# Kernel tuning notes

Hardware: AMD Instinct MI355X
Metric: run time of the kernel (lower is better)

## Reference

```python
import jax, jax.numpy as jnp
import numpy as np

FORGET_BIAS = 1.0  # tf LSTMCell default

def _lstm_step(c, h, xt, W, b):
    # tf LSTMCell: gates = [x, h] @ W + b, split order (i, j, f, o)
    gates = jnp.concatenate([xt, h], axis=-1) @ W + b
    i, j, f, o = jnp.split(gates, 4, axis=-1)
    c_new = c * jax.nn.sigmoid(f + FORGET_BIAS) + jax.nn.sigmoid(i) * jnp.tanh(j)
    h_new = jnp.tanh(c_new) * jax.nn.sigmoid(o)
    return c_new, h_new

def setup_inputs() -> dict:
    key = jax.random.key(0)
    k1, k2, k3 = jax.random.split(key, 3)
    B, T, H = 512, 1024, 64
    x = jax.random.normal(k1, (B, T, 1), dtype=jnp.float32)
    W1 = jax.random.normal(k2, (1 + H, 4 * H), dtype=jnp.float32) * 0.1
    b1 = jnp.zeros((4 * H,), dtype=jnp.float32)
    W2 = jax.random.normal(k3, (H + 1, 4 * 1), dtype=jnp.float32) * 0.1
    b2 = jnp.zeros((4,), dtype=jnp.float32)
    return {"x": x, "W1": W1, "b1": b1, "W2": W2, "b2": b2}

def reference(x, W1, b1, W2, b2):
    B, T, _ = x.shape
    H = W1.shape[1] // 4
    xs = jnp.swapaxes(x, 0, 1)  # [T, B, 1]

    def step(carry, xt):
        c1, h1, c2, h2 = carry
        c1, h1 = _lstm_step(c1, h1, xt, W1, b1)   # layer 1: in=1, hidden=64
        c2, h2 = _lstm_step(c2, h2, h1, W2, b2)   # layer 2: in=64, hidden=1
        return (c1, h1, c2, h2), h2

    init = (jnp.zeros((B, H), x.dtype), jnp.zeros((B, H), x.dtype),
            jnp.zeros((B, 1), x.dtype), jnp.zeros((B, 1), x.dtype))
    _, ys = jax.lax.scan(step, init, xs)  # ys: [T, B, 1]
    return jnp.swapaxes(ys, 0, 1)  # [B, T, 1]
```

## Files before the change

### kernel.cpp

```cpp
#include <hip/hip_runtime.h>


#define TT 1024

__device__ __forceinline__ float fsig(float x) {
    return __builtin_amdgcn_rcpf(1.f + __expf(-x));
}
__device__ __forceinline__ float ftanh(float x) {
    return 1.f - 2.f * __builtin_amdgcn_rcpf(1.f + __expf(2.f * x));
}

template <int Ctrl, int Rmask>
__device__ __forceinline__ float dpp_add(float x) {
    int t = __builtin_amdgcn_update_dpp(0, __float_as_int(x), Ctrl, Rmask, 0xf, true);
    return x + __int_as_float(t);
}
__device__ __forceinline__ float wave_sum64(float x) {
    x = dpp_add<0x111, 0xf>(x);
    x = dpp_add<0x112, 0xf>(x);
    x = dpp_add<0x114, 0xf>(x);
    x = dpp_add<0x118, 0xf>(x);
    x = dpp_add<0x142, 0xa>(x);
    x = dpp_add<0x143, 0xc>(x);
    return x;
}

__global__ __launch_bounds__(576) void lstm2_kernel(
    const float* __restrict__ x,
    const float* __restrict__ W1,
    const float* __restrict__ b1,
    const float* __restrict__ W2,
    const float* __restrict__ b2,
    float* __restrict__ y)
{
    __shared__ __align__(16) float xs[TT];
    __shared__ __align__(16) float h1s[64];
    __shared__ __align__(16) float gs[2][4][64];
    __shared__ float dbuf[2][4];

    const int tid  = threadIdx.x;
    const int b    = blockIdx.x;
    const int lane = tid & 63;
    const int cw   = tid >> 6;
    const int half = lane >> 5;
    const int l31  = lane & 31;
    const int col  = (cw << 5) | l31;
    const int g    = cw >> 1;

    if (tid < 256) {
        ((float4*)xs)[tid] = ((const float4*)(x + (size_t)b * TT))[tid];
    }

    float w[33];
    float bias = 0.f, w2g = 0.f;
    if (cw < 8) {
        if (half == 0) {
            w[0] = W1[col];
            bias = b1[col];
#pragma unroll
            for (int j = 1; j <= 32; ++j) w[j] = W1[j * 256 + col];
        } else {
            w[0] = 0.f;
#pragma unroll
            for (int j = 1; j <= 32; ++j) w[j] = W1[(32 + j) * 256 + col];
        }
    }
    if (cw < 4) w2g = W2[lane * 4 + cw];

    const float w2h0 = W2[256], w2h1 = W2[257], w2h2 = W2[258], w2h3 = W2[259];
    const float b20 = b2[0], b21 = b2[1], b22 = b2[2], b23 = b2[3];

    float c1 = 0.f;
    float c2 = 0.f, h2 = 0.f;

    if (tid < 64) h1s[tid] = 0.f;
    __syncthreads();

    float* yrow = y + (size_t)b * TT;
    const int hbase = half << 3;

    for (int t = 0; t < TT; ++t) {
        const int par = t & 1;
        if (cw < 8) {
            const float xt = xs[t];
            float a0 = fmaf(xt, w[0], bias), a1 = 0.f, a2 = 0.f, a3 = 0.f;
#pragma unroll
            for (int q = 0; q < 8; ++q) {
                float4 h4 = ((const float4*)h1s)[hbase + q];
                a0 = fmaf(h4.x, w[1 + 4*q], a0);
                a1 = fmaf(h4.y, w[2 + 4*q], a1);
                a2 = fmaf(h4.z, w[3 + 4*q], a2);
                a3 = fmaf(h4.w, w[4 + 4*q], a3);
            }
            float p = (a0 + a1) + (a2 + a3);
            p += __shfl_xor(p, 32);
            float act;
            if (g == 1)      act = ftanh(p);
            else if (g == 2) act = fsig(p + 1.f);
            else             act = fsig(p);
            if (half == 0) gs[par][g][(cw & 1) * 32 + l31] = act;
        }
        __syncthreads();
        if (cw < 8) {
            const float i_ = gs[par][0][lane], j_ = gs[par][1][lane];
            const float f_ = gs[par][2][lane], o_ = gs[par][3][lane];
            c1 = fmaf(c1, f_, i_ * j_);
            const float h1 = ftanh(c1) * o_;
            h1s[lane] = h1;
            if (cw < 4) {
                float p = wave_sum64(h1 * w2g);
                if (lane == 63) dbuf[par][cw] = p;
            }
        } else if (t > 0 && lane == 0) {
            const int pp = par ^ 1;
            const float d0 = dbuf[pp][0], d1 = dbuf[pp][1];
            const float d2 = dbuf[pp][2], d3 = dbuf[pp][3];
            const float i2 = fsig (fmaf(h2, w2h0, d0) + b20);
            const float j2 = ftanh(fmaf(h2, w2h1, d1) + b21);
            const float f2 = fsig (fmaf(h2, w2h2, d2) + b22 + 1.f);
            const float o2 = fsig (fmaf(h2, w2h3, d3) + b23);
            c2 = fmaf(c2, f2, i2 * j2);
            h2 = ftanh(c2) * o2;
            yrow[t - 1] = h2;
        }
    }
    __syncthreads();
    if (cw == 8 && lane == 0) {
        const int pp = (TT - 1) & 1;
        const float d0 = dbuf[pp][0], d1 = dbuf[pp][1];
        const float d2 = dbuf[pp][2], d3 = dbuf[pp][3];
        const float i2 = fsig (fmaf(h2, w2h0, d0) + b20);
        const float j2 = ftanh(fmaf(h2, w2h1, d1) + b21);
        const float f2 = fsig (fmaf(h2, w2h2, d2) + b22 + 1.f);
        const float o2 = fsig (fmaf(h2, w2h3, d3) + b23);
        c2 = fmaf(c2, f2, i2 * j2);
        h2 = ftanh(c2) * o2;
        yrow[TT - 1] = h2;
    }
}

extern "C" void kernel_launch(void* const* d_in, const int* in_sizes, int n_in,
                              void* d_out, int out_size, void* d_ws, size_t ws_size,
                              hipStream_t stream) {
    const float* x  = (const float*)d_in[0];
    const float* W1 = (const float*)d_in[1];
    const float* b1 = (const float*)d_in[2];
    const float* W2 = (const float*)d_in[3];
    const float* b2 = (const float*)d_in[4];
    float* y = (float*)d_out;
    lstm2_kernel<<<512, 576, 0, stream>>>(x, W1, b1, W2, b2, y);
}
```

Baseline: 779.1 us.

## Cut LSTM step to one barrier with double-buffered h1 and wave-specialized layer 2

Double-buffers the h1 state so each timestep needs a single block barrier instead of two. Stores gates interleaved per unit so each hidden unit reads its four gates with one float4 load. Computes activations branch-free with one exp2/rcp formula, and unrolls the time loop by four with a vector load of x. Moves the whole layer-2 reduction into the ninth wave, which does four wave sums per step, and adds an occupancy hint to launch bounds. The barrier counts in the two wave-specialized branches must stay matched, which makes the code fragile, and the layer-2 wave now does more serial work per step.

New measurement: 696.6 us. 10.6% less time.

```diff
diff --git a/kernel.cpp b/kernel.cpp
--- a/kernel.cpp
+++ b/kernel.cpp
@@ -25,7 +25,7 @@
     return x;
 }
 
-__global__ __launch_bounds__(576) void lstm2_kernel(
+__global__ __launch_bounds__(576, 6) void lstm2_kernel(
     const float* __restrict__ x,
     const float* __restrict__ W1,
     const float* __restrict__ b1,
@@ -34,9 +34,8 @@
     float* __restrict__ y)
 {
     __shared__ __align__(16) float xs[TT];
-    __shared__ __align__(16) float h1s[64];
-    __shared__ __align__(16) float gs[2][4][64];
-    __shared__ float dbuf[2][4];
+    __shared__ __align__(16) float h1s[2][64];
+    __shared__ __align__(16) float gs[2][64][4];
 
     const int tid  = threadIdx.x;
     const int b    = blockIdx.x;
@@ -44,16 +43,21 @@
     const int cw   = tid >> 6;
     const int half = lane >> 5;
     const int l31  = lane & 31;
-    const int col  = (cw << 5) | l31;
-    const int g    = cw >> 1;
 
     if (tid < 256) {
         ((float4*)xs)[tid] = ((const float4*)(x + (size_t)b * TT))[tid];
     }
+    if (tid < 128) ((float*)h1s)[tid] = 0.f;
 
-    float w[33];
-    float bias = 0.f, w2g = 0.f;
+    float* yrow = y + (size_t)b * TT;
+
     if (cw < 8) {
+        const int col   = (cw << 5) | l31;
+        const int g     = cw >> 1;
+        const int gunit = ((cw & 1) << 5) | l31;
+
+        float w[33];
+        float bias = 0.f;
         if (half == 0) {
             w[0] = W1[col];
             bias = b1[col];
@@ -64,78 +68,91 @@
 #pragma unroll
             for (int j = 1; j <= 32; ++j) w[j] = W1[(32 + j) * 256 + col];
         }
-    }
-    if (cw < 4) w2g = W2[lane * 4 + cw];
 
-    const float w2h0 = W2[256], w2h1 = W2[257], w2h2 = W2[258], w2h3 = W2[259];
-    const float b20 = b2[0], b21 = b2[1], b22 = b2[2], b23 = b2[3];
+        const float L2E = 1.4426950408889634f;
+        const float mm = (g == 1) ? 2.f * L2E : -L2E;
+        const float kk = (g == 2) ? -L2E : 0.f;
+        const float aa = (g == 1) ? 1.f : 0.f;
+        const float bb = (g == 1) ? -2.f : 1.f;
 
-    float c1 = 0.f;
-    float c2 = 0.f, h2 = 0.f;
+        const int hrow = half << 3;
+        float c1 = 0.f;
+        __syncthreads();
 
-    if (tid < 64) h1s[tid] = 0.f;
-    __syncthreads();
+#define STEP(PAR, XT) { \
+        float a0 = fmaf((XT), w[0], bias), a1 = 0.f, a2 = 0.f, a3 = 0.f; \
+        const float4* hb = (const float4*)(&h1s[(PAR) ^ 1][0]); \
+        _Pragma("unroll") \
+        for (int q = 0; q < 8; ++q) { \
+            float4 h4 = hb[hrow + q]; \
+            a0 = fmaf(h4.x, w[1 + 4 * q], a0); \
+            a1 = fmaf(h4.y, w[2 + 4 * q], a1); \
+            a2 = fmaf(h4.z, w[3 + 4 * q], a2); \
+            a3 = fmaf(h4.w, w[4 + 4 * q], a3); \
+        } \
+        float p = (a0 + a1) + (a2 + a3); \
+        p += __shfl_xor(p, 32); \
+        float act = fmaf(bb, __builtin_amdgcn_rcpf(1.f + exp2f(fmaf(mm, p, kk))), aa); \
+        gs[PAR][gunit][g] = act; \
+        __syncthreads(); \
+        float4 g4 = *(const float4*)(&gs[PAR][lane][0]); \
+        c1 = fmaf(c1, g4.z, g4.x * g4.y); \
+        float rr = __builtin_amdgcn_rcpf(1.f + exp2f(c1 * (2.f * L2E))); \
+        float tt_ = rr * g4.w; \
+        h1s[PAR][lane] = fmaf(-2.f, tt_, g4.w); }
 
-    float* yrow = y + (size_t)b * TT;
-    const int hbase = half << 3;
+        for (int t = 0; t < TT; t += 4) {
+            float4 x4 = *(const float4*)(xs + t);
+            STEP(0, x4.x)
+            STEP(1, x4.y)
+            STEP(0, x4.z)
+            STEP(1, x4.w)
+        }
+#undef STEP
+        __syncthreads();
+    } else {
+        float4 w2g4 = *(const float4*)(W2 + lane * 4);
+        const float w2h0 = W2[256], w2h1 = W2[257], w2h2 = W2[258], w2h3 = W2[259];
+        const float b20 = b2[0], b21 = b2[1], b22 = b2[2], b23 = b2[3];
+        float c2 = 0.f, h2 = 0.f;
+        __syncthreads();
 
-    for (int t = 0; t < TT; ++t) {
-        const int par = t & 1;
-        if (cw < 8) {
-            const float xt = xs[t];
-            float a0 = fmaf(xt, w[0], bias), a1 = 0.f, a2 = 0.f, a3 = 0.f;
-#pragma unroll
-            for (int q = 0; q < 8; ++q) {
-                float4 h4 = ((const float4*)h1s)[hbase + q];
-                a0 = fmaf(h4.x, w[1 + 4*q], a0);
-                a1 = fmaf(h4.y, w[2 + 4*q], a1);
-                a2 = fmaf(h4.z, w[3 + 4*q], a2);
-                a3 = fmaf(h4.w, w[4 + 4*q], a3);
+        for (int t = 0; t < TT; ++t) {
+            __syncthreads();
+            if (t > 0) {
+                const float hv = h1s[(t - 1) & 1][lane];
+                const float d0 = wave_sum64(hv * w2g4.x);
+                const float d1 = wave_sum64(hv * w2g4.y);
+                const float d2 = wave_sum64(hv * w2g4.z);
+                const float d3 = wave_sum64(hv * w2g4.w);
+                if (lane == 63) {
+                    const float i2 = fsig (fmaf(h2, w2h0, d0) + b20);
+                    const float j2 = ftanh(fmaf(h2, w2h1, d1) + b21);
+                    const float f2 = fsig (fmaf(h2, w2h2, d2) + b22 + 1.f);
+                    const float o2 = fsig (fmaf(h2, w2h3, d3) + b23);
+                    c2 = fmaf(c2, f2, i2 * j2);
+                    h2 = ftanh(c2) * o2;
+                    yrow[t - 1] = h2;
+                }
             }
-            float p = (a0 + a1) + (a2 + a3);
-            p += __shfl_xor(p, 32);
-            float act;
-            if (g == 1)      act = ftanh(p);
-            else if (g == 2) act = fsig(p + 1.f);
-            else             act = fsig(p);
-            if (half == 0) gs[par][g][(cw & 1) * 32 + l31] = act;
         }
         __syncthreads();
-        if (cw < 8) {
-            const float i_ = gs[par][0][lane], j_ = gs[par][1][lane];
-            const float f_ = gs[par][2][lane], o_ = gs[par][3][lane];
-            c1 = fmaf(c1, f_, i_ * j_);
-            const float h1 = ftanh(c1) * o_;
-            h1s[lane] = h1;
-            if (cw < 4) {
-                float p = wave_sum64(h1 * w2g);
-                if (lane == 63) dbuf[par][cw] = p;
+        {
+            const float hv = h1s[(TT - 1) & 1][lane];
+            const float d0 = wave_sum64(hv * w2g4.x);
+            const float d1 = wave_sum64(hv * w2g4.y);
+            const float d2 = wave_sum64(hv * w2g4.z);
+            const float d3 = wave_sum64(hv * w2g4.w);
+            if (lane == 63) {
+                const float i2 = fsig (fmaf(h2, w2h0, d0) + b20);
+                const float j2 = ftanh(fmaf(h2, w2h1, d1) + b21);
+                const float f2 = fsig (fmaf(h2, w2h2, d2) + b22 + 1.f);
+                const float o2 = fsig (fmaf(h2, w2h3, d3) + b23);
+                c2 = fmaf(c2, f2, i2 * j2);
+                h2 = ftanh(c2) * o2;
+                yrow[TT - 1] = h2;
             }
-        } else if (t > 0 && lane == 0) {
-            const int pp = par ^ 1;
-            const float d0 = dbuf[pp][0], d1 = dbuf[pp][1];
-            const float d2 = dbuf[pp][2], d3 = dbuf[pp][3];
-            const float i2 = fsig (fmaf(h2, w2h0, d0) + b20);
-            const float j2 = ftanh(fmaf(h2, w2h1, d1) + b21);
-            const float f2 = fsig (fmaf(h2, w2h2, d2) + b22 + 1.f);
-            const float o2 = fsig (fmaf(h2, w2h3, d3) + b23);
-            c2 = fmaf(c2, f2, i2 * j2);
-            h2 = ftanh(c2) * o2;
-            yrow[t - 1] = h2;
         }
-    }
-    __syncthreads();
-    if (cw == 8 && lane == 0) {
-        const int pp = (TT - 1) & 1;
-        const float d0 = dbuf[pp][0], d1 = dbuf[pp][1];
-        const float d2 = dbuf[pp][2], d3 = dbuf[pp][3];
-        const float i2 = fsig (fmaf(h2, w2h0, d0) + b20);
-        const float j2 = ftanh(fmaf(h2, w2h1, d1) + b21);
-        const float f2 = fsig (fmaf(h2, w2h2, d2) + b22 + 1.f);
-        const float o2 = fsig (fmaf(h2, w2h3, d3) + b23);
-        c2 = fmaf(c2, f2, i2 * j2);
-        h2 = ftanh(c2) * o2;
-        yrow[TT - 1] = h2;
     }
 }
 
```
